# Kernel optimization log

Measured on AMD Instinct MI355X. Metric: run time of the kernel, lower is better.

The kernel has to match this reference:

```python
import jax, jax.numpy as jnp
import numpy as np

B, T, N, E = 4, 12, 2000, 32000
ND, ED = 16, 8
H, D = 4, 16
G = H * D          # gat_hidden = 64
GH = 64            # gru_hidden
LN_EPS = 1e-5


def setup_inputs() -> dict:
    key = jax.random.key(0)
    ks = jax.random.split(key, 12)

    def xavier(k, shape):
        fan_in, fan_out = shape[0], shape[-1]
        lim = np.sqrt(6.0 / (fan_in + fan_out))
        return jax.random.uniform(k, shape, jnp.float32, -lim, lim)

    return {
        "node_features": jax.random.normal(ks[0], (B, T, N, ND), jnp.float32),
        "edge_features": jax.random.normal(ks[1], (B, T, E, ED), jnp.float32),
        "W_node": xavier(ks[2], (ND, G)),
        "W_edge": xavier(ks[3], (ED, G)),
        "att": xavier(ks[4], (H, 3 * D)),
        "ln_gamma": jnp.ones((G,), jnp.float32),
        "ln_beta": jnp.zeros((G,), jnp.float32),
        "W_ih": xavier(ks[5], (3 * GH, G)),
        "W_hh": xavier(ks[6], (3 * GH, GH)),
        "b_ih": jnp.zeros((3 * GH,), jnp.float32),
        "b_hh": jnp.zeros((3 * GH,), jnp.float32),
        "W_out": xavier(ks[7], (GH, 1)),
        "b_out": jnp.zeros((1,), jnp.float32),
        "edge_index": jax.random.randint(ks[8], (2, E), 0, N).astype(jnp.int64),
    }


def reference(node_features, edge_features, W_node, W_edge, att, ln_gamma,
              ln_beta, W_ih, W_hh, b_ih, b_hh, W_out, b_out, edge_index):
    Bv, Tv, Nv, _ = node_features.shape
    Ev = edge_features.shape[2]
    Hv = att.shape[0]
    Dv = att.shape[1] // 3
    Gv = Hv * Dv
    src, dst = edge_index[0], edge_index[1]
    a_dst, a_src, a_e = att[:, :Dv], att[:, Dv:2 * Dv], att[:, 2 * Dv:]

    def gat_single(x, ea):
        # x: [N, ND], ea: [E, ED]
        h = (x @ W_node).reshape(Nv, Hv, Dv)          # [N,H,D]
        e = (ea @ W_edge).reshape(Ev, Hv, Dv)          # [E,H,D]
        # score = LeakyReLU(a . [h_dst | h_src | e]) — compute per-node parts
        # at node level then gather (same math, avoids [E,H,3D] concat).
        s_d = jnp.einsum('nhd,hd->nh', h, a_dst)       # [N,H]
        s_s = jnp.einsum('nhd,hd->nh', h, a_src)       # [N,H]
        s_e = jnp.einsum('ehd,hd->eh', e, a_e)         # [E,H]
        score = jax.nn.leaky_relu(s_d[dst] + s_s[src] + s_e, 0.2)  # [E,H]
        # segment softmax over in-neighbours of dst
        smax = jax.ops.segment_max(score, dst, num_segments=Nv)
        exp_s = jnp.exp(score - smax[dst])
        ssum = jax.ops.segment_sum(exp_s, dst, num_segments=Nv)
        alpha = exp_s / (ssum[dst] + 1e-16)            # [E,H]
        msg = h[src] + e                               # [E,H,D]
        out = jax.ops.segment_sum(alpha[..., None] * msg, dst,
                                  num_segments=Nv)     # [N,H,D]
        out = jax.nn.elu(out).reshape(Nv, Gv)
        mu = out.mean(-1, keepdims=True)
        var = ((out - mu) ** 2).mean(-1, keepdims=True)
        out = (out - mu) / jnp.sqrt(var + LN_EPS) * ln_gamma + ln_beta
        return out, alpha

    # vmap over the B*T independent graph instances
    x_flat = node_features.reshape(Bv * Tv, Nv, -1)
    e_flat = edge_features.reshape(Bv * Tv, Ev, -1)
    gat_out, alpha_all = jax.vmap(gat_single)(x_flat, e_flat)
    spatial = gat_out.reshape(Bv, Tv, Nv, Gv)
    attn_stack = alpha_all.reshape(Bv, Tv, Ev, Hv).mean(axis=0)  # [T,E,H]

    # GRU over T (batch_first, single layer)
    gru_in = spatial.transpose(0, 2, 1, 3).reshape(Bv * Nv, Tv, Gv)
    xs = gru_in.transpose(1, 0, 2)  # [T, B*N, G]

    def gru_step(hprev, x):
        gi = x @ W_ih.T + b_ih
        gh = hprev @ W_hh.T + b_hh
        i_r, i_z, i_n = jnp.split(gi, 3, axis=-1)
        h_r, h_z, h_n = jnp.split(gh, 3, axis=-1)
        r = jax.nn.sigmoid(i_r + h_r)
        z = jax.nn.sigmoid(i_z + h_z)
        n = jnp.tanh(i_n + r * h_n)
        hnew = (1.0 - z) * n + z * hprev
        return hnew, None

    h0 = jnp.zeros((Bv * Nv, W_hh.shape[1]), gru_in.dtype)
    h_last, _ = jax.lax.scan(gru_step, h0, xs)
    h_i = h_last.reshape(Bv, Nv, -1)               # [B,N,GH]
    pred = h_i @ W_out + b_out                     # [B,N,1]
    return pred, h_i, attn_stack
```

## Files before the change

kernel.cpp:

```cpp
#include <hip/hip_runtime.h>
#include <hip/hip_bf16.h>
#include <math.h>
#include <stdint.h>

#define BQ 4
#define TQ 12
#define NQ 2000
#define EQ 32000
#define NDQ 16
#define EDQ 8
#define HQ 4
#define DQ 16
#define GQ 64
#define GHQ 64
#define NGQ 48
#define LN_EPSQ 1e-5f
#define CCAP 64
#define ATTN_OFF 520000

typedef _Float16 half8 __attribute__((ext_vector_type(8)));
typedef _Float16 half4v __attribute__((ext_vector_type(4)));
typedef float f32x4 __attribute__((ext_vector_type(4)));

__global__ void k_count(const int* __restrict__ ei, int* __restrict__ count) {
    int e = blockIdx.x * blockDim.x + threadIdx.x;
    if (e < EQ) atomicAdd(&count[ei[EQ + e]], 1);
}

__global__ void k_scan(const int* __restrict__ count, int* __restrict__ offs,
                       int* __restrict__ cursor) {
    __shared__ int buf[2][2048];
    int t = threadIdx.x;
    for (int i = t; i < 2048; i += 1024)
        buf[0][i] = (i < NQ) ? count[i] : 0;
    __syncthreads();
    int src = 0;
    for (int sh = 1; sh < 2048; sh <<= 1) {
        int dst = src ^ 1;
        for (int i = t; i < 2048; i += 1024) {
            int v = buf[src][i];
            if (i >= sh) v += buf[src][i - sh];
            buf[dst][i] = v;
        }
        __syncthreads();
        src = dst;
    }
    for (int i = t; i <= NQ; i += 1024) {
        int off = (i == 0) ? 0 : buf[src][i - 1];
        offs[i] = off;
        if (i < NQ) cursor[i] = off;
    }
}

__global__ void k_scatter(const int* __restrict__ ei, int* __restrict__ cursor,
                          int2* __restrict__ csr2) {
    int e = blockIdx.x * blockDim.x + threadIdx.x;
    if (e < EQ) {
        int pos = atomicAdd(&cursor[ei[EQ + e]], 1);
        csr2[pos] = make_int2(e, ei[e]);
    }
}

__global__ void __launch_bounds__(256) k_nodeproj(
        const float* __restrict__ xf, const float* __restrict__ Wn,
        const float* __restrict__ att,
        _Float16* __restrict__ hprojH, float* __restrict__ sd,
        float* __restrict__ ss) {
    __shared__ __align__(16) float4 Wl4[NDQ * 16];
    __shared__ float attl[HQ * 48];
    int t = threadIdx.x;
    for (int i = t; i < NDQ * 16; i += 256) Wl4[i] = ((const float4*)Wn)[i];
    if (t < HQ * 48) attl[t] = att[t];
    __syncthreads();
    int id = blockIdx.x * 256 + t;
    const float4* xp = (const float4*)(xf + (size_t)id * NDQ);
    float4 xv0 = xp[0], xv1 = xp[1], xv2 = xp[2], xv3 = xp[3];
    float xr[16] = {xv0.x, xv0.y, xv0.z, xv0.w, xv1.x, xv1.y, xv1.z, xv1.w,
                    xv2.x, xv2.y, xv2.z, xv2.w, xv3.x, xv3.y, xv3.z, xv3.w};
    float acc[64];
#pragma unroll
    for (int j = 0; j < 64; ++j) acc[j] = 0.f;
#pragma unroll
    for (int i = 0; i < 16; ++i) {
        float xi = xr[i];
#pragma unroll
        for (int j4 = 0; j4 < 16; ++j4) {
            float4 wv = Wl4[i * 16 + j4];
            acc[j4 * 4 + 0] = fmaf(xi, wv.x, acc[j4 * 4 + 0]);
            acc[j4 * 4 + 1] = fmaf(xi, wv.y, acc[j4 * 4 + 1]);
            acc[j4 * 4 + 2] = fmaf(xi, wv.z, acc[j4 * 4 + 2]);
            acc[j4 * 4 + 3] = fmaf(xi, wv.w, acc[j4 * 4 + 3]);
        }
    }
    float sdv[4], ssv[4];
#pragma unroll
    for (int hh = 0; hh < 4; ++hh) {
        float vd = 0.f, vs = 0.f;
#pragma unroll
        for (int d = 0; d < 16; ++d) {
            vd = fmaf(acc[hh * 16 + d], attl[hh * 48 + d], vd);
            vs = fmaf(acc[hh * 16 + d], attl[hh * 48 + 16 + d], vs);
        }
        sdv[hh] = vd; ssv[hh] = vs;
    }
    *(float4*)&sd[(size_t)id * 4] = make_float4(sdv[0], sdv[1], sdv[2], sdv[3]);
    *(float4*)&ss[(size_t)id * 4] = make_float4(ssv[0], ssv[1], ssv[2], ssv[3]);
#pragma unroll
    for (int p = 0; p < 8; ++p) {
        half8 hv;
#pragma unroll
        for (int i = 0; i < 8; ++i) hv[i] = (_Float16)acc[p * 8 + i];
        *(half8*)&hprojH[(size_t)id * GQ + p * 8] = hv;
    }
}

__global__ void __launch_bounds__(256) k_fused(
        const float* __restrict__ ef, const float* __restrict__ We,
        const float* __restrict__ att,
        const int* __restrict__ offs, const int2* __restrict__ csr2,
        const float* __restrict__ sd, const float* __restrict__ ss,
        const _Float16* __restrict__ hprojH,
        const float* __restrict__ gamma, const float* __restrict__ beta,
        _Float16* __restrict__ alphaH, _Float16* __restrict__ spatialH) {
    __shared__ float Wl[EDQ * GQ];
    __shared__ __align__(16) float WA[EDQ * HQ];
    __shared__ __align__(16) float ecache[4][CCAP * 4];
    __shared__ half8 eac[4][CCAP];
    __shared__ int   srcs[4][CCAP];
    __shared__ int   eids[4][CCAP];
    int t = threadIdx.x;
    for (int i = t; i < EDQ * GQ; i += 256) Wl[i] = We[i];
    if (t < EDQ * HQ) {
        int i = t >> 2, h4 = t & 3;
        float s = 0.f;
#pragma unroll
        for (int d = 0; d < DQ; ++d)
            s = fmaf(We[i * GQ + h4 * DQ + d], att[h4 * 48 + 32 + d], s);
        WA[t] = s;
    }
    __syncthreads();
    int w = t >> 6, lane = t & 63;
    int wid = blockIdx.x * 4 + w;
    int g = wid / NQ, n = wid % NQ;
    int beg = offs[n], deg = offs[n + 1] - beg;
    size_t ebase = (size_t)g * EQ;
    size_t nbase = (size_t)g * NQ;
    float4 sd4 = *(const float4*)&sd[(nbase + n) * HQ];
    float mxr[4] = {-1e30f, -1e30f, -1e30f, -1e30f};
    for (int k = lane; k < deg; k += 64) {
        int2 pr = csr2[beg + k];
        float4 ssv = *(const float4*)&ss[(nbase + pr.y) * HQ];
        const float4* eap = (const float4*)(ef + (ebase + pr.x) * EDQ);
        float4 lo = eap[0], hi = eap[1];
        float scv[4];
#pragma unroll
        for (int hh = 0; hh < 4; ++hh) {
            float se =      lo.x * WA[0 * 4 + hh];
            se = fmaf(lo.y, WA[1 * 4 + hh], se); se = fmaf(lo.z, WA[2 * 4 + hh], se);
            se = fmaf(lo.w, WA[3 * 4 + hh], se); se = fmaf(hi.x, WA[4 * 4 + hh], se);
            se = fmaf(hi.y, WA[5 * 4 + hh], se); se = fmaf(hi.z, WA[6 * 4 + hh], se);
            se = fmaf(hi.w, WA[7 * 4 + hh], se);
            float sdh = (hh == 0) ? sd4.x : (hh == 1) ? sd4.y : (hh == 2) ? sd4.z : sd4.w;
            float ssh = (hh == 0) ? ssv.x : (hh == 1) ? ssv.y : (hh == 2) ? ssv.z : ssv.w;
            float sc = sdh + ssh + se;
            sc = (sc >= 0.f) ? sc : 0.2f * sc;
            scv[hh] = sc;
            mxr[hh] = fmaxf(mxr[hh], sc);
        }
        if (k < CCAP) {
            *(float4*)&ecache[w][k * 4] = make_float4(scv[0], scv[1], scv[2], scv[3]);
            half8 hv;
            hv[0] = (_Float16)lo.x; hv[1] = (_Float16)lo.y;
            hv[2] = (_Float16)lo.z; hv[3] = (_Float16)lo.w;
            hv[4] = (_Float16)hi.x; hv[5] = (_Float16)hi.y;
            hv[6] = (_Float16)hi.z; hv[7] = (_Float16)hi.w;
            eac[w][k] = hv;
            srcs[w][k] = pr.y;
            eids[w][k] = pr.x;
        }
    }
#pragma unroll
    for (int s = 1; s < 64; s <<= 1) {
#pragma unroll
        for (int hh = 0; hh < 4; ++hh)
            mxr[hh] = fmaxf(mxr[hh], __shfl_xor(mxr[hh], s, 64));
    }
    int h = lane >> 4, c = lane & 15;
    float mxh = (h == 0) ? mxr[0] : (h == 1) ? mxr[1] : (h == 2) ? mxr[2] : mxr[3];
    float sdh = (h == 0) ? sd4.x : (h == 1) ? sd4.y : (h == 2) ? sd4.z : sd4.w;
    float sum = 0.f;
    float ws[8] = {0.f, 0.f, 0.f, 0.f, 0.f, 0.f, 0.f, 0.f};
    for (int k = c; k < deg; k += 16) {
        float e;
        if (k < CCAP) {
            e = __expf(ecache[w][k * 4 + h] - mxh);
            ecache[w][k * 4 + h] = e;
            half8 ev = eac[w][k];
#pragma unroll
            for (int i = 0; i < 8; ++i) ws[i] = fmaf(e, (float)ev[i], ws[i]);
        } else {
            int2 pr = csr2[beg + k];
            float4 ssv = *(const float4*)&ss[(nbase + pr.y) * HQ];
            float ssh = (h == 0) ? ssv.x : (h == 1) ? ssv.y : (h == 2) ? ssv.z : ssv.w;
            const float4* eap = (const float4*)(ef + (ebase + pr.x) * EDQ);
            float4 lo = eap[0], hi = eap[1];
            float se =      lo.x * WA[0 * 4 + h];
            se = fmaf(lo.y, WA[1 * 4 + h], se); se = fmaf(lo.z, WA[2 * 4 + h], se);
            se = fmaf(lo.w, WA[3 * 4 + h], se); se = fmaf(hi.x, WA[4 * 4 + h], se);
            se = fmaf(hi.y, WA[5 * 4 + h], se); se = fmaf(hi.z, WA[6 * 4 + h], se);
            se = fmaf(hi.w, WA[7 * 4 + h], se);
            float sc = sdh + ssh + se;
            sc = (sc >= 0.f) ? sc : 0.2f * sc;
            e = __expf(sc - mxh);
            ws[0] = fmaf(e, lo.x, ws[0]); ws[1] = fmaf(e, lo.y, ws[1]);
            ws[2] = fmaf(e, lo.z, ws[2]); ws[3] = fmaf(e, lo.w, ws[3]);
            ws[4] = fmaf(e, hi.x, ws[4]); ws[5] = fmaf(e, hi.y, ws[5]);
            ws[6] = fmaf(e, hi.z, ws[6]); ws[7] = fmaf(e, hi.w, ws[7]);
        }
        sum += e;
    }
#pragma unroll
    for (int s = 1; s < 16; s <<= 1) {
        sum += __shfl_xor(sum, s, 16);
#pragma unroll
        for (int i = 0; i < 8; ++i) ws[i] += __shfl_xor(ws[i], s, 16);
    }
    float inv = 1.f / (sum + 1e-16f);
#pragma unroll
    for (int i = 0; i < 8; ++i) ws[i] *= inv;
    for (int k = c; k < deg; k += 16) {
        float e; int eid;
        if (k < CCAP) {
            e = ecache[w][k * 4 + h];
            eid = eids[w][k];
        } else {
            int2 pr = csr2[beg + k];
            eid = pr.x;
            float4 ssv = *(const float4*)&ss[(nbase + pr.y) * HQ];
            float ssh = (h == 0) ? ssv.x : (h == 1) ? ssv.y : (h == 2) ? ssv.z : ssv.w;
            const float4* eap = (const float4*)(ef + (ebase + pr.x) * EDQ);
            float4 lo = eap[0], hi = eap[1];
            float se =      lo.x * WA[0 * 4 + h];
            se = fmaf(lo.y, WA[1 * 4 + h], se); se = fmaf(lo.z, WA[2 * 4 + h], se);
            se = fmaf(lo.w, WA[3 * 4 + h], se); se = fmaf(hi.x, WA[4 * 4 + h], se);
            se = fmaf(hi.y, WA[5 * 4 + h], se); se = fmaf(hi.z, WA[6 * 4 + h], se);
            se = fmaf(hi.w, WA[7 * 4 + h], se);
            float sc = sdh + ssh + se;
            sc = (sc >= 0.f) ? sc : 0.2f * sc;
            e = __expf(sc - mxh);
        }
        alphaH[(ebase + eid) * HQ + h] = (_Float16)(e * inv);
    }
    int dmain = deg < CCAP ? deg : CCAP;
    const _Float16* hp = hprojH + nbase * GQ + lane;
    float acc = 0.f;
    int k = 0;
    for (; k + 8 <= dmain; k += 8) {
        float e0 = ecache[w][(k + 0) * 4 + h], e1 = ecache[w][(k + 1) * 4 + h];
        float e2 = ecache[w][(k + 2) * 4 + h], e3 = ecache[w][(k + 3) * 4 + h];
        float e4 = ecache[w][(k + 4) * 4 + h], e5 = ecache[w][(k + 5) * 4 + h];
        float e6 = ecache[w][(k + 6) * 4 + h], e7 = ecache[w][(k + 7) * 4 + h];
        float h0 = (float)hp[(size_t)srcs[w][k + 0] * GQ];
        float h1 = (float)hp[(size_t)srcs[w][k + 1] * GQ];
        float h2 = (float)hp[(size_t)srcs[w][k + 2] * GQ];
        float h3 = (float)hp[(size_t)srcs[w][k + 3] * GQ];
        float h4 = (float)hp[(size_t)srcs[w][k + 4] * GQ];
        float h5 = (float)hp[(size_t)srcs[w][k + 5] * GQ];
        float h6 = (float)hp[(size_t)srcs[w][k + 6] * GQ];
        float h7 = (float)hp[(size_t)srcs[w][k + 7] * GQ];
        acc = fmaf(e0, h0, acc); acc = fmaf(e1, h1, acc);
        acc = fmaf(e2, h2, acc); acc = fmaf(e3, h3, acc);
        acc = fmaf(e4, h4, acc); acc = fmaf(e5, h5, acc);
        acc = fmaf(e6, h6, acc); acc = fmaf(e7, h7, acc);
    }
    for (; k < dmain; ++k) {
        float e0 = ecache[w][k * 4 + h];
        float h0 = (float)hp[(size_t)srcs[w][k] * GQ];
        acc = fmaf(e0, h0, acc);
    }
    for (; k < deg; ++k) {
        int2 pr = csr2[beg + k];
        float4 ssv = *(const float4*)&ss[(nbase + pr.y) * HQ];
        float ssh = (h == 0) ? ssv.x : (h == 1) ? ssv.y : (h == 2) ? ssv.z : ssv.w;
        const float4* eap = (const float4*)(ef + (ebase + pr.x) * EDQ);
        float4 lo = eap[0], hi = eap[1];
        float se =      lo.x * WA[0 * 4 + h];
        se = fmaf(lo.y, WA[1 * 4 + h], se); se = fmaf(lo.z, WA[2 * 4 + h], se);
        se = fmaf(lo.w, WA[3 * 4 + h], se); se = fmaf(hi.x, WA[4 * 4 + h], se);
        se = fmaf(hi.y, WA[5 * 4 + h], se); se = fmaf(hi.z, WA[6 * 4 + h], se);
        se = fmaf(hi.w, WA[7 * 4 + h], se);
        float sc = sdh + ssh + se;
        sc = (sc >= 0.f) ? sc : 0.2f * sc;
        float e0 = __expf(sc - mxh);
        float h0 = (float)hp[(size_t)pr.y * GQ];
        acc = fmaf(e0, h0, acc);
    }
    acc *= inv;
    float t2 = 0.f;
#pragma unroll
    for (int i = 0; i < 8; ++i) t2 = fmaf(ws[i], Wl[i * GQ + lane], t2);
    float x = acc + t2;
    x = (x > 0.f) ? x : (__expf(x) - 1.f);
    float s1 = x, s2v = x * x;
#pragma unroll
    for (int s = 32; s >= 1; s >>= 1) {
        s1 += __shfl_xor(s1, s, 64);
        s2v += __shfl_xor(s2v, s, 64);
    }
    float mu = s1 * (1.f / 64.f);
    float var = s2v * (1.f / 64.f) - mu * mu;
    float y = (x - mu) * rsqrtf(var + LN_EPSQ) * gamma[lane] + beta[lane];
    spatialH[(nbase + n) * GQ + lane] = (_Float16)y;
}

__device__ inline f32x4 MF(half8 a, half8 b, f32x4 c) {
    return __builtin_amdgcn_mfma_f32_16x16x32_f16(a, b, c, 0, 0, 0);
}

__global__ void __launch_bounds__(256) k_gru(
        const _Float16* __restrict__ xh,
        const float* __restrict__ Wih, const float* __restrict__ Whh,
        const float* __restrict__ bih, const float* __restrict__ bhh,
        const float* __restrict__ Wout, const float* __restrict__ bout,
        float* __restrict__ out) {
    __shared__ _Float16 hlds[16][72];
    __shared__ float pred_s[4][16];
    int tid = threadIdx.x;
    int w = tid >> 6, l = tid & 63;
    int lr = l & 15, lg = l >> 4;
    int j = w * 16 + lr;
    half8 wiF[3][2], whF[3][2];
#pragma unroll
    for (int gb = 0; gb < 3; ++gb) {
        int q = gb * 64 + j;
#pragma unroll
        for (int kt = 0; kt < 2; ++kt) {
            const float* p  = Wih + q * 64 + kt * 32 + lg * 8;
            const float* p2 = Whh + q * 64 + kt * 32 + lg * 8;
            half8 a, b;
#pragma unroll
            for (int i = 0; i < 8; ++i) { a[i] = (_Float16)p[i]; b[i] = (_Float16)p2[i]; }
            wiF[gb][kt] = a; whF[gb][kt] = b;
        }
    }
    float br  = bih[j] + bhh[j];
    float bz  = bih[64 + j] + bhh[64 + j];
    float bin = bih[128 + j];
    float bhn = bhh[128 + j];
    float wo  = Wout[j];
    for (int i = tid; i < 16 * 72; i += 256) ((_Float16*)hlds)[i] = (_Float16)0.f;
    int id0 = blockIdx.x * 16;
    const _Float16* xp0;
    {
        int id = id0 + lr;
        int b = id / NQ, n = id - b * NQ;
        xp0 = xh + ((size_t)b * TQ * NQ + n) * GQ + lg * 8;
    }
    half8 xa[2];
    xa[0] = *(const half8*)xp0; xa[1] = *(const half8*)(xp0 + 32);
    float hprev[4] = {0.f, 0.f, 0.f, 0.f};
    __syncthreads();
    for (int t = 0; t < TQ; ++t) {
        f32x4 aR  = (f32x4){br, br, br, br};
        f32x4 aZ  = (f32x4){bz, bz, bz, bz};
        f32x4 aIN = (f32x4){bin, bin, bin, bin};
        f32x4 aHN = (f32x4){bhn, bhn, bhn, bhn};
#pragma unroll
        for (int kt = 0; kt < 2; ++kt) {
            aR  = MF(xa[kt], wiF[0][kt], aR);
            aZ  = MF(xa[kt], wiF[1][kt], aZ);
            aIN = MF(xa[kt], wiF[2][kt], aIN);
        }
        half8 ha[2];
        ha[0] = *(const half8*)&hlds[lr][lg * 8];
        ha[1] = *(const half8*)&hlds[lr][32 + lg * 8];
#pragma unroll
        for (int kt = 0; kt < 2; ++kt) {
            aR  = MF(ha[kt], whF[0][kt], aR);
            aZ  = MF(ha[kt], whF[1][kt], aZ);
            aHN = MF(ha[kt], whF[2][kt], aHN);
        }
        if (t + 1 < TQ) {
            xp0 += (size_t)NQ * GQ;
            xa[0] = *(const half8*)xp0; xa[1] = *(const half8*)(xp0 + 32);
        }
#pragma unroll
        for (int r4 = 0; r4 < 4; ++r4) {
            float r = 1.f / (1.f + __expf(-aR[r4]));
            float z = 1.f / (1.f + __expf(-aZ[r4]));
            float xg = aIN[r4] + r * aHN[r4];
            float e2 = __expf(2.f * xg);
            float nn = 1.f - 2.f / (e2 + 1.f);
            hprev[r4] = z * (hprev[r4] - nn) + nn;
        }
        __syncthreads();
#pragma unroll
        for (int r4 = 0; r4 < 4; ++r4)
            hlds[4 * lg + r4][j] = (_Float16)hprev[r4];
        __syncthreads();
    }
    float pv[4];
#pragma unroll
    for (int r4 = 0; r4 < 4; ++r4) {
        int id = id0 + 4 * lg + r4;
        out[8000 + (size_t)id * GHQ + j] = hprev[r4];
        pv[r4] = hprev[r4] * wo;
    }
#pragma unroll
    for (int s = 1; s <= 8; s <<= 1)
#pragma unroll
        for (int r4 = 0; r4 < 4; ++r4)
            pv[r4] += __shfl_xor(pv[r4], s);
    if (lr == 0) {
#pragma unroll
        for (int r4 = 0; r4 < 4; ++r4)
            pred_s[w][4 * lg + r4] = pv[r4];
    }
    __syncthreads();
    if (tid < 16) {
        float s = pred_s[0][tid] + pred_s[1][tid] + pred_s[2][tid] + pred_s[3][tid] + bout[0];
        out[id0 + tid] = s;
    }
}

__global__ void k_attn(const _Float16* __restrict__ alpha, float* __restrict__ out) {
    int gid = blockIdx.x * blockDim.x + threadIdx.x;
    if (gid >= TQ * EQ) return;
    int tt = gid / EQ, e = gid % EQ;
    float a0 = 0.f, a1 = 0.f, a2 = 0.f, a3 = 0.f;
#pragma unroll
    for (int b = 0; b < BQ; ++b) {
        half4v v = *(const half4v*)&alpha[(((size_t)b * TQ + tt) * EQ + e) * HQ];
        a0 += (float)v[0]; a1 += (float)v[1]; a2 += (float)v[2]; a3 += (float)v[3];
    }
    float4 r = {a0 * 0.25f, a1 * 0.25f, a2 * 0.25f, a3 * 0.25f};
    *(float4*)&out[ATTN_OFF + (size_t)gid * HQ] = r;
}

extern "C" void kernel_launch(void* const* d_in, const int* in_sizes, int n_in,
                              void* d_out, int out_size, void* d_ws, size_t ws_size,
                              hipStream_t stream) {
    const float* nodef = (const float*)d_in[0];
    const float* edgef = (const float*)d_in[1];
    const float* Wn    = (const float*)d_in[2];
    const float* We    = (const float*)d_in[3];
    const float* att   = (const float*)d_in[4];
    const float* gamma = (const float*)d_in[5];
    const float* beta  = (const float*)d_in[6];
    const float* Wih   = (const float*)d_in[7];
    const float* Whh   = (const float*)d_in[8];
    const float* bih   = (const float*)d_in[9];
    const float* bhh   = (const float*)d_in[10];
    const float* Wout  = (const float*)d_in[11];
    const float* bout  = (const float*)d_in[12];
    const int*   ei    = (const int*)d_in[13];

    char* ws = (char*)d_ws;
    size_t o = 0;
    int*  count  = (int*)(ws + o);  o += 2048 * 4;
    int*  offs   = (int*)(ws + o);  o += 2048 * 4;
    int*  cursor = (int*)(ws + o);  o += 2048 * 4;
    int2* csr2   = (int2*)(ws + o); o += (size_t)EQ * 8;
    float* sd      = (float*)(ws + o); o += (size_t)NGQ * NQ * HQ * 4;
    float* ss      = (float*)(ws + o); o += (size_t)NGQ * NQ * HQ * 4;
    _Float16* hprojH   = (_Float16*)(ws + o); o += (size_t)NGQ * NQ * GQ * 2;
    _Float16* alphaH   = (_Float16*)(ws + o); o += (size_t)NGQ * EQ * HQ * 2;
    _Float16* spatialH = (_Float16*)(ws + o); o += (size_t)NGQ * NQ * GQ * 2;

    hipMemsetAsync(count, 0, NQ * sizeof(int), stream);
    k_count  <<<(EQ + 255) / 256, 256, 0, stream>>>(ei, count);
    k_scan   <<<1, 1024, 0, stream>>>(count, offs, cursor);
    k_scatter<<<(EQ + 255) / 256, 256, 0, stream>>>(ei, cursor, csr2);

    k_nodeproj<<<(NGQ * NQ) / 256, 256, 0, stream>>>(nodef, Wn, att, hprojH, sd, ss);
    k_fused   <<<(NGQ * NQ) / 4, 256, 0, stream>>>(edgef, We, att, offs, csr2,
                                                   sd, ss, hprojH, gamma, beta,
                                                   alphaH, spatialH);
    k_gru     <<<(BQ * NQ) / 16, 256, 0, stream>>>(spatialH, Wih, Whh, bih, bhh,
                                                   Wout, bout, (float*)d_out);
    k_attn    <<<(TQ * EQ + 255) / 256, 256, 0, stream>>>(alphaH, (float*)d_out);
}
```

Before: 284.1 us.

## Merge CSR build into one block kernel and fold attention mean into GRU

Replaces the memset, count, scan and scatter launches with a single 1024-thread block that counts, scans and scatters entirely in shared memory. It also removes the separate attention-averaging kernel and moves that work into the tail of the GRU kernel: each of the 500 GRU blocks averages 768 edge-time entries. The goal is fewer kernel launches and less launch and dependency overhead. In exchange the CSR build runs serially on one CU, and the GRU blocks carry extra memory traffic.

New measurement: 305.8 us. 1.08x slower.

```diff
diff --git a/kernel.cpp b/kernel.cpp
--- a/kernel.cpp
+++ b/kernel.cpp
@@ -22,17 +22,18 @@
 typedef _Float16 half4v __attribute__((ext_vector_type(4)));
 typedef float f32x4 __attribute__((ext_vector_type(4)));
 
-__global__ void k_count(const int* __restrict__ ei, int* __restrict__ count) {
-    int e = blockIdx.x * blockDim.x + threadIdx.x;
-    if (e < EQ) atomicAdd(&count[ei[EQ + e]], 1);
-}
-
-__global__ void k_scan(const int* __restrict__ count, int* __restrict__ offs,
-                       int* __restrict__ cursor) {
+__global__ void __launch_bounds__(1024) k_csr(const int* __restrict__ ei,
+                                              int* __restrict__ offs,
+                                              int2* __restrict__ csr2) {
+    __shared__ int cnt[2048];
     __shared__ int buf[2][2048];
+    __shared__ int cur[2048];
     int t = threadIdx.x;
-    for (int i = t; i < 2048; i += 1024)
-        buf[0][i] = (i < NQ) ? count[i] : 0;
+    for (int i = t; i < 2048; i += 1024) cnt[i] = 0;
+    __syncthreads();
+    for (int e = t; e < EQ; e += 1024) atomicAdd(&cnt[ei[EQ + e]], 1);
+    __syncthreads();
+    for (int i = t; i < 2048; i += 1024) buf[0][i] = cnt[i];
     __syncthreads();
     int src = 0;
     for (int sh = 1; sh < 2048; sh <<= 1) {
@@ -48,15 +49,12 @@
     for (int i = t; i <= NQ; i += 1024) {
         int off = (i == 0) ? 0 : buf[src][i - 1];
         offs[i] = off;
-        if (i < NQ) cursor[i] = off;
-    }
-}
-
-__global__ void k_scatter(const int* __restrict__ ei, int* __restrict__ cursor,
-                          int2* __restrict__ csr2) {
-    int e = blockIdx.x * blockDim.x + threadIdx.x;
-    if (e < EQ) {
-        int pos = atomicAdd(&cursor[ei[EQ + e]], 1);
+        if (i < NQ) cur[i] = off;
+    }
+    __syncthreads();
+    for (int e = t; e < EQ; e += 1024) {
+        int d = ei[EQ + e];
+        int pos = atomicAdd(&cur[d], 1);
         csr2[pos] = make_int2(e, ei[e]);
     }
 }
@@ -322,6 +320,7 @@
         const float* __restrict__ Wih, const float* __restrict__ Whh,
         const float* __restrict__ bih, const float* __restrict__ bhh,
         const float* __restrict__ Wout, const float* __restrict__ bout,
+        const _Float16* __restrict__ alphaH,
         float* __restrict__ out) {
     __shared__ _Float16 hlds[16][72];
     __shared__ float pred_s[4][16];
@@ -421,20 +420,18 @@
         float s = pred_s[0][tid] + pred_s[1][tid] + pred_s[2][tid] + pred_s[3][tid] + bout[0];
         out[id0 + tid] = s;
     }
-}
-
-__global__ void k_attn(const _Float16* __restrict__ alpha, float* __restrict__ out) {
-    int gid = blockIdx.x * blockDim.x + threadIdx.x;
-    if (gid >= TQ * EQ) return;
-    int tt = gid / EQ, e = gid % EQ;
-    float a0 = 0.f, a1 = 0.f, a2 = 0.f, a3 = 0.f;
-#pragma unroll
-    for (int b = 0; b < BQ; ++b) {
-        half4v v = *(const half4v*)&alpha[(((size_t)b * TQ + tt) * EQ + e) * HQ];
-        a0 += (float)v[0]; a1 += (float)v[1]; a2 += (float)v[2]; a3 += (float)v[3];
-    }
-    float4 r = {a0 * 0.25f, a1 * 0.25f, a2 * 0.25f, a3 * 0.25f};
-    *(float4*)&out[ATTN_OFF + (size_t)gid * HQ] = r;
+#pragma unroll
+    for (int q = 0; q < 3; ++q) {
+        int gid = blockIdx.x * 768 + q * 256 + tid;
+        float a0 = 0.f, a1 = 0.f, a2 = 0.f, a3 = 0.f;
+#pragma unroll
+        for (int b = 0; b < BQ; ++b) {
+            half4v v = *(const half4v*)&alphaH[((size_t)b * (TQ * EQ) + gid) * HQ];
+            a0 += (float)v[0]; a1 += (float)v[1]; a2 += (float)v[2]; a3 += (float)v[3];
+        }
+        float4 r = {a0 * 0.25f, a1 * 0.25f, a2 * 0.25f, a3 * 0.25f};
+        *(float4*)&out[ATTN_OFF + (size_t)gid * HQ] = r;
+    }
 }
 
 extern "C" void kernel_launch(void* const* d_in, const int* in_sizes, int n_in,
@@ -457,9 +454,7 @@
 
     char* ws = (char*)d_ws;
     size_t o = 0;
-    int*  count  = (int*)(ws + o);  o += 2048 * 4;
     int*  offs   = (int*)(ws + o);  o += 2048 * 4;
-    int*  cursor = (int*)(ws + o);  o += 2048 * 4;
     int2* csr2   = (int2*)(ws + o); o += (size_t)EQ * 8;
     float* sd      = (float*)(ws + o); o += (size_t)NGQ * NQ * HQ * 4;
     float* ss      = (float*)(ws + o); o += (size_t)NGQ * NQ * HQ * 4;
@@ -467,16 +462,11 @@
     _Float16* alphaH   = (_Float16*)(ws + o); o += (size_t)NGQ * EQ * HQ * 2;
     _Float16* spatialH = (_Float16*)(ws + o); o += (size_t)NGQ * NQ * GQ * 2;
 
-    hipMemsetAsync(count, 0, NQ * sizeof(int), stream);
-    k_count  <<<(EQ + 255) / 256, 256, 0, stream>>>(ei, count);
-    k_scan   <<<1, 1024, 0, stream>>>(count, offs, cursor);
-    k_scatter<<<(EQ + 255) / 256, 256, 0, stream>>>(ei, cursor, csr2);
-
+    k_csr     <<<1, 1024, 0, stream>>>(ei, offs, csr2);
     k_nodeproj<<<(NGQ * NQ) / 256, 256, 0, stream>>>(nodef, Wn, att, hprojH, sd, ss);
     k_fused   <<<(NGQ * NQ) / 4, 256, 0, stream>>>(edgef, We, att, offs, csr2,
                                                    sd, ss, hprojH, gamma, beta,
                                                    alphaH, spatialH);
     k_gru     <<<(BQ * NQ) / 16, 256, 0, stream>>>(spatialH, Wih, Whh, bih, bhh,
-                                                   Wout, bout, (float*)d_out);
-    k_attn    <<<(TQ * EQ + 255) / 256, 256, 0, stream>>>(alphaH, (float*)d_out);
-}
+                                                   Wout, bout, alphaH, (float*)d_out);
+}
```
